# Kernel optimization log

Hardware: AMD Instinct MI355X
Metric: run time of the kernel (lower is better)

Reference implementation:

```python
import jax, jax.numpy as jnp
import numpy as np

PAD_IDX = 0
EPS = 1e-5


def make_pos(L):
    # phrase[i, j] = j - i, i.e. row i is range(-i, L-i)
    phrase = (np.arange(L)[None, :] - np.arange(L)[:, None]).astype(np.float32)
    half = int(np.ceil(L / 2))
    freq = np.linspace(0.0, L, L, dtype=np.float32)[1:half]          # [F]
    pos = freq[:, None, None] * phrase[None] / L * 2.0 * np.pi       # [F, L, L]
    pos = np.concatenate([np.cos(pos), np.sin(pos)], axis=0)        # [2F, L, L]
    return jnp.asarray(np.transpose(pos, (1, 0, 2)))                # [L, P=2F, L]


def setup_inputs() -> dict:
    key = jax.random.key(0)
    ks = jax.random.split(key, 8)
    B, L, V, D, H = 2048, 64, 4096, 64, 8
    P = 2 * (int(np.ceil(L / 2)) - 1)  # 62
    inputs = jax.random.randint(ks[0], (B, L), 0, V)
    W_emb = jax.random.normal(ks[1], (V, D), jnp.float32) * 0.02
    W_emb = W_emb.at[PAD_IDX].set(0.0)  # padding_idx row is zero
    W_qkv = jax.random.normal(ks[2], (3 * H * D, D), jnp.float32) * 0.02
    W_pos = jax.random.normal(ks[3], (P, L), jnp.float32) * 0.02
    ln_g = jnp.ones((D,), jnp.float32)
    ln_b = jnp.zeros((D,), jnp.float32)
    W1 = jax.random.normal(ks[4], (64, H), jnp.float32) * 0.1
    b1 = jnp.zeros((64,), jnp.float32)
    W2 = jax.random.normal(ks[5], (32, 64), jnp.float32) * 0.1
    b2 = jnp.zeros((32,), jnp.float32)
    return dict(inputs=inputs, W_emb=W_emb, W_qkv=W_qkv, W_pos=W_pos,
                ln_g=ln_g, ln_b=ln_b, W1=W1, b1=b1, W2=W2, b2=b2,
                n_words=4, n_names=16)


def reference(inputs, W_emb, W_qkv, W_pos, ln_g, ln_b, W1, b1, W2, b2, n_words, n_names):
    B, L = inputs.shape
    V, D = W_emb.shape
    H = W_qkv.shape[0] // (3 * D)
    pos = make_pos(L)  # [L, P, L]
    P = pos.shape[1]

    # compute_qkv: per-char q/k/v tables, then gather per token.
    qkv = (W_emb @ W_qkv.T).reshape(V, 3 * H, D)
    q, k, v = qkv[:, :H], qkv[:, H:2 * H], qkv[:, 2 * H:]
    q_t = jnp.take(q, inputs, axis=0)  # [B, L, H, D]
    k_t = jnp.take(k, inputs, axis=0)
    v_t = jnp.take(v, inputs, axis=0)

    # Equivalent to gathering char_sim[h, ids, ids]: qkv is a per-token linear,
    # so q[ids] @ k[ids]^T == char_sim.index_select(1, ids).index_select(-1, ids).
    sim = jnp.einsum('blhd,bmhd->bhlm', q_t, k_t) / jnp.sqrt(jnp.float32(D))
    key_pad = (inputs == PAD_IDX)[:, None, None, :]
    sim = jnp.where(key_pad, jnp.float32(-1e9), sim)  # char_sim[:, :, pad_idx] = -1e9

    # positional bias: Linear(L->P) on clipped scores, contracted with pos basis.
    sim_clip = jnp.where(sim > -1e8, sim, jnp.float32(0.0))
    pos_w = jnp.einsum('bhlm,pm->bhlp', sim_clip, W_pos)        # [B, H, L, P]
    pos_bias = jnp.einsum('bhlp,lpm->bhlm', pos_w, pos) / P     # mean over P

    attn = jax.nn.softmax(sim + pos_bias, axis=-1)              # dropout p=0 -> id
    out = jnp.einsum('bhlm,bmhd->blhd', attn, v_t)              # [B, L, H, D]

    # sdpa LayerNorm over word_vec_d
    mu = out.mean(-1, keepdims=True)
    var = out.var(-1, keepdims=True)
    out = (out - mu) * jax.lax.rsqrt(var + EPS) * ln_g + ln_b

    # MLP over the head dimension: [B, L, D, H] -> [B, L, D, 32]
    ft = jnp.swapaxes(out, 2, 3)
    h1 = jax.nn.relu(jnp.einsum('bldh,oh->bldo', ft, W1) + b1)
    h2 = jnp.einsum('bldo,po->bldp', h1, W2) + b2
    char_ft = h2.reshape(B, L, -1)                              # [B, L, D*32]

    # masked mean pooling over chars -> word feature
    maskf = (inputs != PAD_IDX).astype(char_ft.dtype)
    word_ft = jnp.einsum('bl,blf->bf', maskf, char_ft) / maskf.sum(-1, keepdims=True)

    # equal-size splits: words -> names (mean) -> groups of names
    Fdim = word_ft.shape[-1]
    name_ft = word_ft.reshape(B // n_words, n_words, Fdim).mean(1)
    return name_ft.reshape(-1, n_names, Fdim)
```

## Files before the change

kernel.cpp:

```cpp
#include <hip/hip_runtime.h>
#include <hip/hip_bf16.h>


typedef __attribute__((ext_vector_type(8))) short short8;
typedef __attribute__((ext_vector_type(4))) float f32x4;

union FragU { uint4 u; short8 v; };

__device__ __forceinline__ unsigned short f2bf(float f) {
    union { float f; unsigned int i; } c; c.f = f;
    unsigned int i = c.i;
    unsigned int r = (i + 0x7fffu + ((i >> 16) & 1u)) >> 16;
    return (unsigned short)r;
}
__device__ __forceinline__ float asf(unsigned int u) {
    union { unsigned int i; float f; } c; c.i = u; return c.f;
}
__device__ __forceinline__ float bfsel(uint2 g, int i) {
    unsigned u = (i < 2) ? g.x : g.y;
    return asf((i & 1) ? (u & 0xffff0000u) : (u << 16));
}

__device__ __forceinline__ void packstore4(unsigned* rowptr, int c,
                                           float v0, float v1, float v2, float v3) {
    float p0 = __shfl_xor(v0, 1), p1 = __shfl_xor(v1, 1);
    float p2 = __shfl_xor(v2, 1), p3 = __shfl_xor(v3, 1);
    int odd = c & 1;
    unsigned a0 = odd ? ((unsigned)f2bf(p2) | ((unsigned)f2bf(v2) << 16))
                      : ((unsigned)f2bf(v0) | ((unsigned)f2bf(p0) << 16));
    unsigned a1 = odd ? ((unsigned)f2bf(p3) | ((unsigned)f2bf(v3) << 16))
                      : ((unsigned)f2bf(v1) | ((unsigned)f2bf(p1) << 16));
    int ba = (c >> 1) + (odd ? 16 : 0);
    rowptr[ba] = a0; rowptr[ba + 8] = a1;
}

__global__ __launch_bounds__(256) void k_qkv(const float* __restrict__ W_emb,
                                             const float* __restrict__ W_qkv,
                                             unsigned short* __restrict__ qkvb) {
    __shared__ float At[4096];
    __shared__ float Bt[4096];
    int t = threadIdx.x;
    int bt = blockIdx.x / 24, rt = blockIdx.x - bt * 24;
    int r = t >> 2, part = t & 3;
    const float4* esrc = (const float4*)(W_emb + (size_t)((bt << 6) + r) * 64 + part * 16);
    const float4* wsrc = (const float4*)(W_qkv + (size_t)((rt << 6) + r) * 64 + part * 16);
#pragma unroll
    for (int j = 0; j < 4; ++j) {
        float4 e4 = esrc[j], w4 = wsrc[j];
        int c0 = part * 16 + j * 4;
        At[(c0 + 0) * 64 + r] = e4.x; At[(c0 + 1) * 64 + r] = e4.y;
        At[(c0 + 2) * 64 + r] = e4.z; At[(c0 + 3) * 64 + r] = e4.w;
        Bt[(c0 + 0) * 64 + r] = w4.x; Bt[(c0 + 1) * 64 + r] = w4.y;
        Bt[(c0 + 2) * 64 + r] = w4.z; Bt[(c0 + 3) * 64 + r] = w4.w;
    }
    __syncthreads();
    int l0 = (t >> 4) << 2, m0 = (t & 15) << 2;
    float acc[4][4] = {};
#pragma unroll 4
    for (int k = 0; k < 64; ++k) {
        float4 a  = *(const float4*)(At + k * 64 + l0);
        float4 bb = *(const float4*)(Bt + k * 64 + m0);
        float aa[4] = {a.x, a.y, a.z, a.w};
        float bv[4] = {bb.x, bb.y, bb.z, bb.w};
#pragma unroll
        for (int i = 0; i < 4; ++i)
#pragma unroll
            for (int j = 0; j < 4; ++j)
                acc[i][j] = fmaf(aa[i], bv[j], acc[i][j]);
    }
#pragma unroll
    for (int i = 0; i < 4; ++i) {
        unsigned w0 = (unsigned)f2bf(acc[i][0]) | ((unsigned)f2bf(acc[i][1]) << 16);
        unsigned w1 = (unsigned)f2bf(acc[i][2]) | ((unsigned)f2bf(acc[i][3]) << 16);
        unsigned* dst = (unsigned*)(qkvb + (size_t)((bt << 6) + l0 + i) * 1536 + (rt << 6) + m0);
        dst[0] = w0; dst[1] = w1;
    }
}

__global__ void k_tab(const float* __restrict__ W_pos,
                      unsigned short* __restrict__ cst,
                      unsigned short* __restrict__ csl,
                      unsigned short* __restrict__ wpos) {
    int t = threadIdx.x;
    const float w = 6.283185307179586f / 63.0f;
    for (int e = t; e < 4096; e += 256) {
        int row = e >> 6, col = e & 63;
        {
            int j = col, x = row;
            float val = 0.0f;
            if (j < 31)       val = cosf(w * (float)(((j + 1) * x) % 63));
            else if (j >= 32 && j < 63) val = sinf(w * (float)(((j - 31) * x) % 63));
            cst[e] = f2bf(val);
        }
        {
            int j = row, x = col;
            float val = 0.0f;
            if (j < 31)       val = cosf(w * (float)(((j + 1) * x) % 63));
            else if (j >= 32 && j < 63) val = sinf(w * (float)(((j - 31) * x) % 63));
            csl[e] = f2bf(val);
        }
        {
            int j = row;
            float val = 0.0f;
            if (j < 31) val = W_pos[j * 64 + col];
            else if (j >= 32 && j < 63) val = W_pos[(j - 1) * 64 + col];
            wpos[e] = f2bf(val);
        }
    }
}

__global__ __launch_bounds__(128, 4) void k_attn(
    const int* __restrict__ inputs,
    const unsigned short* __restrict__ qkvb,
    const unsigned short* __restrict__ cstg,
    const unsigned short* __restrict__ cslg,
    const unsigned short* __restrict__ wposg,
    const float* __restrict__ ln_g,
    const float* __restrict__ ln_b,
    unsigned short* __restrict__ out_n)
{
    __shared__ __align__(16) unsigned int smem[4608];
    unsigned int* S0d = smem;
    unsigned int* S1d = smem + 2304;
    int t = threadIdx.x, w2 = t >> 6, lane = t & 63;
    int b = blockIdx.x >> 3, h = blockIdx.x & 7;
    const int* toks = inputs + b * 64;
    int r = lane & 15, q = lane >> 4, c = r;
    int tk = toks[lane];
    int mt0 = 2 * w2;

    int mk[4]; float gvv[4], bvv[4];
#pragma unroll
    for (int nt = 0; nt < 4; ++nt) {
        mk[nt] = (toks[16 * nt + c] == 0);
        gvv[nt] = ln_g[16 * nt + c];
        bvv[nt] = ln_b[16 * nt + c];
    }

    {
        const uint4* src = (const uint4*)(qkvb + (size_t)tk * 1536 + (w2 ? 512 : 0) + h * 64);
        uint4* dst = (uint4*)((w2 ? S1d : S0d) + lane * 36);
#pragma unroll
        for (int j = 0; j < 8; ++j) dst[j] = src[j];
    }
    __syncthreads();

    f32x4 sc[2][4], acc[2][4];
    const f32x4 zf = {0.f, 0.f, 0.f, 0.f};

#pragma unroll
    for (int u = 0; u < 2; ++u)
#pragma unroll
        for (int nt = 0; nt < 4; ++nt) sc[u][nt] = zf;
#pragma unroll
    for (int ks = 0; ks < 2; ++ks) {
        FragU Af[2], Bf[4];
#pragma unroll
        for (int u = 0; u < 2; ++u)
            Af[u].u = *(const uint4*)(S0d + (16 * (mt0 + u) + r) * 36 + 16 * ks + 4 * q);
#pragma unroll
        for (int nt = 0; nt < 4; ++nt)
            Bf[nt].u = *(const uint4*)(S1d + (16 * nt + r) * 36 + 16 * ks + 4 * q);
#pragma unroll
        for (int u = 0; u < 2; ++u)
#pragma unroll
            for (int nt = 0; nt < 4; ++nt)
                sc[u][nt] = __builtin_amdgcn_mfma_f32_16x16x32_bf16(Af[u].v, Bf[nt].v, sc[u][nt], 0, 0, 0);
    }
#pragma unroll
    for (int u = 0; u < 2; ++u) {
#pragma unroll
        for (int nt = 0; nt < 4; ++nt) {
            f32x4 vv = sc[u][nt];
#pragma unroll
            for (int i = 0; i < 4; ++i) vv[i] = mk[nt] ? 0.0f : vv[i] * 0.125f;
            sc[u][nt] = vv;
        }
#pragma unroll
        for (int i = 0; i < 4; ++i) {
            int l = 16 * (mt0 + u) + 4 * q + i;
            packstore4(S0d + l * 36, c, sc[u][0][i], sc[u][1][i], sc[u][2][i], sc[u][3][i]);
        }
    }
    __syncthreads();

#pragma unroll
    for (int u = 0; u < 2; ++u)
#pragma unroll
        for (int nt = 0; nt < 4; ++nt) acc[u][nt] = zf;
#pragma unroll
    for (int ks = 0; ks < 2; ++ks) {
        FragU Af[2], Bf[4];
#pragma unroll
        for (int u = 0; u < 2; ++u)
            Af[u].u = *(const uint4*)(S0d + (16 * (mt0 + u) + r) * 36 + 16 * ks + 4 * q);
#pragma unroll
        for (int nt = 0; nt < 4; ++nt)
            Bf[nt].u = *(const uint4*)(wposg + (16 * nt + r) * 64 + 32 * ks + 8 * q);
#pragma unroll
        for (int u = 0; u < 2; ++u)
#pragma unroll
            for (int nt = 0; nt < 4; ++nt)
                acc[u][nt] = __builtin_amdgcn_mfma_f32_16x16x32_bf16(Af[u].v, Bf[nt].v, acc[u][nt], 0, 0, 0);
    }
#pragma unroll
    for (int u = 0; u < 2; ++u) {
        int mt = mt0 + u;
        uint2 t00 = *(const uint2*)(cslg + (c) * 64 + 16 * mt + 4 * q);
        uint2 t01 = *(const uint2*)(cslg + (32 + c) * 64 + 16 * mt + 4 * q);
        uint2 t10 = *(const uint2*)(cslg + (16 + c) * 64 + 16 * mt + 4 * q);
        uint2 t11 = *(const uint2*)(cslg + (48 + c) * 64 + 16 * mt + 4 * q);
#pragma unroll
        for (int i = 0; i < 4; ++i) {
            int l = 16 * mt + 4 * q + i;
            float cv0 = bfsel(t00, i), sv0 = bfsel(t01, i);
            float cv1 = bfsel(t10, i), sv1 = bfsel(t11, i);
            float pc0 = acc[u][0][i], ps0 = acc[u][2][i];
            float pc1 = acc[u][1][i], ps1 = acc[u][3][i];
            float u0 = pc0 * cv0 - ps0 * sv0;
            float u1 = pc1 * cv1 - ps1 * sv1;
            float u2 = pc0 * sv0 + ps0 * cv0;
            float u3 = pc1 * sv1 + ps1 * cv1;
            packstore4(S1d + l * 36, c, u0, u1, u2, u3);
        }
    }

#pragma unroll
    for (int u = 0; u < 2; ++u)
#pragma unroll
        for (int nt = 0; nt < 4; ++nt) acc[u][nt] = zf;
#pragma unroll
    for (int ks = 0; ks < 2; ++ks) {
        FragU Af[2], Bf[4];
#pragma unroll
        for (int u = 0; u < 2; ++u)
            Af[u].u = *(const uint4*)(S1d + (16 * (mt0 + u) + r) * 36 + 16 * ks + 4 * q);
#pragma unroll
        for (int nt = 0; nt < 4; ++nt)
            Bf[nt].u = *(const uint4*)(cstg + (16 * nt + r) * 64 + 32 * ks + 8 * q);
#pragma unroll
        for (int u = 0; u < 2; ++u)
#pragma unroll
            for (int nt = 0; nt < 4; ++nt)
                acc[u][nt] = __builtin_amdgcn_mfma_f32_16x16x32_bf16(Af[u].v, Bf[nt].v, acc[u][nt], 0, 0, 0);
    }

    uint4 V4[4];
    {
        const uint4* vsrc = (const uint4*)(qkvb + (size_t)tk * 1536 + 1024 + h * 64 + 32 * w2);
#pragma unroll
        for (int j = 0; j < 4; ++j) V4[j] = vsrc[j];
    }

#pragma unroll
    for (int u = 0; u < 2; ++u)
#pragma unroll
        for (int i = 0; i < 4; ++i) {
            int l = 16 * (mt0 + u) + 4 * q + i;
            float e0 = mk[0] ? 0.f : __expf(fmaf(acc[u][0][i], 1.0f / 62.0f, sc[u][0][i]));
            float e1 = mk[1] ? 0.f : __expf(fmaf(acc[u][1][i], 1.0f / 62.0f, sc[u][1][i]));
            float e2 = mk[2] ? 0.f : __expf(fmaf(acc[u][2][i], 1.0f / 62.0f, sc[u][2][i]));
            float e3 = mk[3] ? 0.f : __expf(fmaf(acc[u][3][i], 1.0f / 62.0f, sc[u][3][i]));
            float s = e0 + e1 + e2 + e3;
            s += __shfl_xor(s, 1);
            s += __shfl_xor(s, 2);
            s += __shfl_xor(s, 4);
            s += __shfl_xor(s, 8);
            float inv = 1.0f / s;
            packstore4(S0d + l * 36, c, e0 * inv, e1 * inv, e2 * inv, e3 * inv);
        }

    {
        int odd = lane & 1;
        const unsigned* Vd = (const unsigned*)V4;
#pragma unroll
        for (int jj = 0; jj < 16; ++jj) {
            unsigned my = Vd[jj];
            unsigned pr = __shfl_xor(my, 1);
            unsigned val = odd ? ((pr >> 16) | (my & 0xffff0000u))
                               : ((my & 0xffffu) | (pr << 16));
            S1d[(32 * w2 + 2 * jj + odd) * 36 + (lane >> 1)] = val;
        }
    }
    __syncthreads();

#pragma unroll
    for (int u = 0; u < 2; ++u)
#pragma unroll
        for (int nt = 0; nt < 4; ++nt) acc[u][nt] = zf;
#pragma unroll
    for (int ks = 0; ks < 2; ++ks) {
        FragU Af[2], Bf[4];
#pragma unroll
        for (int u = 0; u < 2; ++u)
            Af[u].u = *(const uint4*)(S0d + (16 * (mt0 + u) + r) * 36 + 16 * ks + 4 * q);
#pragma unroll
        for (int nt = 0; nt < 4; ++nt)
            Bf[nt].u = *(const uint4*)(S1d + (16 * nt + r) * 36 + 16 * ks + 4 * q);
#pragma unroll
        for (int u = 0; u < 2; ++u)
#pragma unroll
            for (int nt = 0; nt < 4; ++nt)
                acc[u][nt] = __builtin_amdgcn_mfma_f32_16x16x32_bf16(Af[u].v, Bf[nt].v, acc[u][nt], 0, 0, 0);
    }
    {
        unsigned* outw = (unsigned*)out_n;
        size_t hb = ((size_t)b * 8 + h) * 64;
#pragma unroll
        for (int u = 0; u < 2; ++u)
#pragma unroll
            for (int i = 0; i < 4; ++i) {
                int l = 16 * (mt0 + u) + 4 * q + i;
                float v0 = acc[u][0][i], v1 = acc[u][1][i], v2 = acc[u][2][i], v3 = acc[u][3][i];
                float s1 = v0 + v1 + v2 + v3;
                float s2 = v0 * v0 + v1 * v1 + v2 * v2 + v3 * v3;
                s1 += __shfl_xor(s1, 1); s2 += __shfl_xor(s2, 1);
                s1 += __shfl_xor(s1, 2); s2 += __shfl_xor(s2, 2);
                s1 += __shfl_xor(s1, 4); s2 += __shfl_xor(s2, 4);
                s1 += __shfl_xor(s1, 8); s2 += __shfl_xor(s2, 8);
                float mu = s1 * (1.0f / 64.0f);
                float var = s2 * (1.0f / 64.0f) - mu * mu;
                float rstd = rsqrtf(var + 1e-5f);
                float y0 = (v0 - mu) * rstd * gvv[0] + bvv[0];
                float y1 = (v1 - mu) * rstd * gvv[1] + bvv[1];
                float y2 = (v2 - mu) * rstd * gvv[2] + bvv[2];
                float y3 = (v3 - mu) * rstd * gvv[3] + bvv[3];
                packstore4(outw + (hb + l) * 32, c, y0, y1, y2, y3);
            }
    }
}

__global__ __launch_bounds__(256) void k_mlp(const int* __restrict__ inputs,
                                             const unsigned short* __restrict__ out_n,
                                             const float* __restrict__ W1,
                                             const float* __restrict__ b1,
                                             float* __restrict__ gws) {
    __shared__ unsigned short XT[8320];
    __shared__ float wl[64];
    int t = threadIdx.x, w = t >> 6, lane = t & 63;
    int b = blockIdx.x;
    int ot = w >> 1, dt = w & 1;
    int kq = lane >> 4, n = lane & 15;

    if (t < 64) {
        int tok = inputs[b * 64 + t];
        unsigned long long bal = __ballot(tok != 0);
        int cnt = __popcll(bal);
        if (cnt < 1) cnt = 1;
        wl[t] = (tok != 0) ? 1.0f / (float)cnt : 0.0f;
    }

    FragU Wf[2];
    float b1v[2];
#pragma unroll
    for (int om = 0; om < 2; ++om) {
        int o = 32 * ot + 16 * om + n;
        b1v[om] = b1[o];
        if (kq == 0) {
            const float4* wsrc = (const float4*)(W1 + o * 8);
            float4 wa = wsrc[0], wb = wsrc[1];
            Wf[om].u.x = (unsigned)f2bf(wa.x) | ((unsigned)f2bf(wa.y) << 16);
            Wf[om].u.y = (unsigned)f2bf(wa.z) | ((unsigned)f2bf(wa.w) << 16);
            Wf[om].u.z = (unsigned)f2bf(wb.x) | ((unsigned)f2bf(wb.y) << 16);
            Wf[om].u.w = (unsigned)f2bf(wb.z) | ((unsigned)f2bf(wb.w) << 16);
        } else {
            Wf[om].u = make_uint4(0, 0, 0, 0);
        }
    }

    f32x4 racc[2][2];
    const f32x4 zf = {0.f, 0.f, 0.f, 0.f};
#pragma unroll
    for (int dm = 0; dm < 2; ++dm)
#pragma unroll
        for (int om = 0; om < 2; ++om) racc[dm][om] = zf;

    int lh = t & 7;
    int lr = (t >> 3) & 15;
    int half = t >> 7;

    for (int cc = 0; cc < 4; ++cc) {
        __syncthreads();
        {
            const unsigned short* src = out_n + (size_t)b * 32768 + lh * 4096
                                        + (16 * cc + lr) * 64 + half * 32;
            unsigned short* dst = XT + lr * 520 + lh;
#pragma unroll
            for (int j = 0; j < 4; ++j) {
                uint4 u = ((const uint4*)src)[j];
                int d0 = half * 32 + j * 8;
                dst[(d0 + 0) * 8] = (unsigned short)(u.x & 0xffffu);
                dst[(d0 + 1) * 8] = (unsigned short)(u.x >> 16);
                dst[(d0 + 2) * 8] = (unsigned short)(u.y & 0xffffu);
                dst[(d0 + 3) * 8] = (unsigned short)(u.y >> 16);
                dst[(d0 + 4) * 8] = (unsigned short)(u.z & 0xffffu);
                dst[(d0 + 5) * 8] = (unsigned short)(u.z >> 16);
                dst[(d0 + 6) * 8] = (unsigned short)(u.w & 0xffffu);
                dst[(d0 + 7) * 8] = (unsigned short)(u.w >> 16);
            }
        }
        __syncthreads();
#pragma unroll 4
        for (int l = 0; l < 16; ++l) {
            FragU Xf[2];
#pragma unroll
            for (int dm = 0; dm < 2; ++dm) {
                if (kq == 0)
                    Xf[dm].u = *(const uint4*)(XT + l * 520 + (32 * dt + 16 * dm + n) * 8);
                else
                    Xf[dm].u = make_uint4(0, 0, 0, 0);
            }
            float wv = wl[16 * cc + l];
#pragma unroll
            for (int dm = 0; dm < 2; ++dm)
#pragma unroll
                for (int om = 0; om < 2; ++om) {
                    f32x4 C = __builtin_amdgcn_mfma_f32_16x16x32_bf16(Xf[dm].v, Wf[om].v, zf, 0, 0, 0);
#pragma unroll
                    for (int i = 0; i < 4; ++i)
                        racc[dm][om][i] = fmaf(wv, fmaxf(C[i] + b1v[om], 0.0f), racc[dm][om][i]);
                }
        }
    }
    float* gb = gws + (size_t)b * 4096;
#pragma unroll
    for (int dm = 0; dm < 2; ++dm)
#pragma unroll
        for (int om = 0; om < 2; ++om) {
            int o = 32 * ot + 16 * om + n;
#pragma unroll
            for (int i = 0; i < 4; ++i) {
                int d = 32 * dt + 16 * dm + 4 * kq + i;
                gb[d * 64 + o] = racc[dm][om][i];
            }
        }
}

__global__ __launch_bounds__(256) void k_final(const float* __restrict__ gws,
                                               const float* __restrict__ W2,
                                               const float* __restrict__ b2,
                                               float* __restrict__ out) {
    __shared__ float gbar[4096];
    __shared__ float w2s[32 * 68];
    __shared__ float b2s[32];
    int t = threadIdx.x;
    int n = blockIdx.x;
    for (int e = t; e < 4096; e += 256) {
        size_t base = (size_t)(4 * n) * 4096 + e;
        gbar[e] = 0.25f * (gws[base] + gws[base + 4096] + gws[base + 8192] + gws[base + 12288]);
    }
    for (int e = t; e < 2048; e += 256) {
        int p = e >> 6, o = e & 63;
        w2s[p * 68 + o] = W2[e];
    }
    if (t < 32) b2s[t] = b2[t];
    __syncthreads();
#pragma unroll
    for (int jj = 0; jj < 8; ++jj) {
        int f = jj * 256 + t;
        int d = f >> 5, p = f & 31;
        float acc = b2s[p];
        for (int o4 = 0; o4 < 16; ++o4) {
            float4 gvv = *(const float4*)(gbar + d * 64 + o4 * 4);
            float4 wv = *(const float4*)(w2s + p * 68 + o4 * 4);
            acc = fmaf(gvv.x, wv.x, acc);
            acc = fmaf(gvv.y, wv.y, acc);
            acc = fmaf(gvv.z, wv.z, acc);
            acc = fmaf(gvv.w, wv.w, acc);
        }
        out[(size_t)n * 2048 + f] = acc;
    }
}

extern "C" void kernel_launch(void* const* d_in, const int* in_sizes, int n_in,
                              void* d_out, int out_size, void* d_ws, size_t ws_size,
                              hipStream_t stream) {
    const int*   inputs = (const int*)d_in[0];
    const float* W_emb  = (const float*)d_in[1];
    const float* W_qkv  = (const float*)d_in[2];
    const float* W_pos  = (const float*)d_in[3];
    const float* ln_g   = (const float*)d_in[4];
    const float* ln_b   = (const float*)d_in[5];
    const float* W1     = (const float*)d_in[6];
    const float* b1     = (const float*)d_in[7];
    const float* W2     = (const float*)d_in[8];
    const float* b2     = (const float*)d_in[9];
    float* out = (float*)d_out;

    unsigned short* qkvb = (unsigned short*)d_ws;
    unsigned short* cst  = qkvb + 6291456;
    unsigned short* csl  = cst + 4096;
    unsigned short* wpos = csl + 4096;
    float* gws = (float*)(wpos + 4096);
    unsigned short* out_n = (unsigned short*)(gws + 8388608);

    hipLaunchKernelGGL(k_qkv,   dim3(64 * 24), dim3(256), 0, stream, W_emb, W_qkv, qkvb);
    hipLaunchKernelGGL(k_tab,   dim3(1),       dim3(256), 0, stream, W_pos, cst, csl, wpos);
    hipLaunchKernelGGL(k_attn,  dim3(16384),   dim3(128), 0, stream,
                       inputs, qkvb, cst, csl, wpos, ln_g, ln_b, out_n);
    hipLaunchKernelGGL(k_mlp,   dim3(2048),    dim3(256), 0, stream, inputs, out_n, W1, b1, gws);
    hipLaunchKernelGGL(k_final, dim3(512),     dim3(256), 0, stream, gws, W2, b2, out);
}
```

Before: 398.6 us.

## Swizzle attention LDS, defer softmax normalization, stage coalesced output, merge prep kernels

Replaces the padded 36-dword LDS row stride in the attention kernel with an XOR-swizzled 32-dword layout, shrinking shared memory and raising the occupancy hint from 4 to 5 blocks. Softmax normalization is deferred: unnormalized exponentials feed the PV MFMA and the row sum is folded into the LayerNorm epsilon, which works because LayerNorm is scale-invariant. The final output is staged through LDS and written with coalesced 16-byte stores instead of scattered 32-bit stores. The table kernel is merged into the QKV kernel as one extra block, removing a launch. It adds an extra barrier and risks small numeric differences from the rescaled epsilon.

```diff
diff --git a/kernel.cpp b/kernel.cpp
--- a/kernel.cpp
+++ b/kernel.cpp
@@ -20,26 +20,68 @@
     unsigned u = (i < 2) ? g.x : g.y;
     return asf((i & 1) ? (u & 0xffff0000u) : (u << 16));
 }
-
-__device__ __forceinline__ void packstore4(unsigned* rowptr, int c,
+__device__ __forceinline__ unsigned pk2(float lo, float hi) {
+    return (unsigned)f2bf(lo) | ((unsigned)f2bf(hi) << 16);
+}
+
+__device__ __forceinline__ int swzi(int row, int dw4) {
+    return (row << 5) + (dw4 ^ ((row & 7) << 2));
+}
+__device__ __forceinline__ int swzs(int row, int dw) {
+    return (row << 5) + (((dw & ~3) ^ ((row & 7) << 2)) | (dw & 3));
+}
+
+__device__ __forceinline__ void packstore4(unsigned* S, int row, int c,
                                            float v0, float v1, float v2, float v3) {
     float p0 = __shfl_xor(v0, 1), p1 = __shfl_xor(v1, 1);
     float p2 = __shfl_xor(v2, 1), p3 = __shfl_xor(v3, 1);
     int odd = c & 1;
-    unsigned a0 = odd ? ((unsigned)f2bf(p2) | ((unsigned)f2bf(v2) << 16))
-                      : ((unsigned)f2bf(v0) | ((unsigned)f2bf(p0) << 16));
-    unsigned a1 = odd ? ((unsigned)f2bf(p3) | ((unsigned)f2bf(v3) << 16))
-                      : ((unsigned)f2bf(v1) | ((unsigned)f2bf(p1) << 16));
+    float x0 = odd ? p2 : v0, y0 = odd ? v2 : p0;
+    float x1 = odd ? p3 : v1, y1 = odd ? v3 : p1;
+    unsigned a0 = pk2(x0, y0), a1 = pk2(x1, y1);
     int ba = (c >> 1) + (odd ? 16 : 0);
-    rowptr[ba] = a0; rowptr[ba + 8] = a1;
-}
-
-__global__ __launch_bounds__(256) void k_qkv(const float* __restrict__ W_emb,
+    S[swzs(row, ba)] = a0;
+    S[swzs(row, ba + 8)] = a1;
+}
+
+__global__ __launch_bounds__(256) void k_pre(const float* __restrict__ W_emb,
                                              const float* __restrict__ W_qkv,
-                                             unsigned short* __restrict__ qkvb) {
+                                             const float* __restrict__ W_pos,
+                                             unsigned short* __restrict__ qkvb,
+                                             unsigned short* __restrict__ cst,
+                                             unsigned short* __restrict__ csl,
+                                             unsigned short* __restrict__ wpos) {
     __shared__ float At[4096];
     __shared__ float Bt[4096];
     int t = threadIdx.x;
+    if (blockIdx.x >= 1536) {
+        const float w = 6.283185307179586f / 63.0f;
+        for (int e = t; e < 4096; e += 256) {
+            int row = e >> 6, col = e & 63;
+            {
+                int j = col, x = row;
+                float val = 0.0f;
+                if (j < 31)       val = cosf(w * (float)(((j + 1) * x) % 63));
+                else if (j >= 32 && j < 63) val = sinf(w * (float)(((j - 31) * x) % 63));
+                cst[e] = f2bf(val);
+            }
+            {
+                int j = row, x = col;
+                float val = 0.0f;
+                if (j < 31)       val = cosf(w * (float)(((j + 1) * x) % 63));
+                else if (j >= 32 && j < 63) val = sinf(w * (float)(((j - 31) * x) % 63));
+                csl[e] = f2bf(val);
+            }
+            {
+                int j = row;
+                float val = 0.0f;
+                if (j < 31) val = W_pos[j * 64 + col];
+                else if (j >= 32 && j < 63) val = W_pos[(j - 1) * 64 + col];
+                wpos[e] = f2bf(val);
+            }
+        }
+        return;
+    }
     int bt = blockIdx.x / 24, rt = blockIdx.x - bt * 24;
     int r = t >> 2, part = t & 3;
     const float4* esrc = (const float4*)(W_emb + (size_t)((bt << 6) + r) * 64 + part * 16);
@@ -70,46 +112,13 @@
     }
 #pragma unroll
     for (int i = 0; i < 4; ++i) {
-        unsigned w0 = (unsigned)f2bf(acc[i][0]) | ((unsigned)f2bf(acc[i][1]) << 16);
-        unsigned w1 = (unsigned)f2bf(acc[i][2]) | ((unsigned)f2bf(acc[i][3]) << 16);
         unsigned* dst = (unsigned*)(qkvb + (size_t)((bt << 6) + l0 + i) * 1536 + (rt << 6) + m0);
-        dst[0] = w0; dst[1] = w1;
-    }
-}
-
-__global__ void k_tab(const float* __restrict__ W_pos,
-                      unsigned short* __restrict__ cst,
-                      unsigned short* __restrict__ csl,
-                      unsigned short* __restrict__ wpos) {
-    int t = threadIdx.x;
-    const float w = 6.283185307179586f / 63.0f;
-    for (int e = t; e < 4096; e += 256) {
-        int row = e >> 6, col = e & 63;
-        {
-            int j = col, x = row;
-            float val = 0.0f;
-            if (j < 31)       val = cosf(w * (float)(((j + 1) * x) % 63));
-            else if (j >= 32 && j < 63) val = sinf(w * (float)(((j - 31) * x) % 63));
-            cst[e] = f2bf(val);
-        }
-        {
-            int j = row, x = col;
-            float val = 0.0f;
-            if (j < 31)       val = cosf(w * (float)(((j + 1) * x) % 63));
-            else if (j >= 32 && j < 63) val = sinf(w * (float)(((j - 31) * x) % 63));
-            csl[e] = f2bf(val);
-        }
-        {
-            int j = row;
-            float val = 0.0f;
-            if (j < 31) val = W_pos[j * 64 + col];
-            else if (j >= 32 && j < 63) val = W_pos[(j - 1) * 64 + col];
-            wpos[e] = f2bf(val);
-        }
-    }
-}
-
-__global__ __launch_bounds__(128, 4) void k_attn(
+        dst[0] = pk2(acc[i][0], acc[i][1]);
+        dst[1] = pk2(acc[i][2], acc[i][3]);
+    }
+}
+
+__global__ __launch_bounds__(128, 5) void k_attn(
     const int* __restrict__ inputs,
     const unsigned short* __restrict__ qkvb,
     const unsigned short* __restrict__ cstg,
@@ -119,9 +128,9 @@
     const float* __restrict__ ln_b,
     unsigned short* __restrict__ out_n)
 {
-    __shared__ __align__(16) unsigned int smem[4608];
+    __shared__ __align__(16) unsigned int smem[4096];
     unsigned int* S0d = smem;
-    unsigned int* S1d = smem + 2304;
+    unsigned int* S1d = smem + 2048;
     int t = threadIdx.x, w2 = t >> 6, lane = t & 63;
     int b = blockIdx.x >> 3, h = blockIdx.x & 7;
     const int* toks = inputs + b * 64;
@@ -139,9 +148,10 @@
 
     {
         const uint4* src = (const uint4*)(qkvb + (size_t)tk * 1536 + (w2 ? 512 : 0) + h * 64);
-        uint4* dst = (uint4*)((w2 ? S1d : S0d) + lane * 36);
-#pragma unroll
-        for (int j = 0; j < 8; ++j) dst[j] = src[j];
+        unsigned* Sd = w2 ? S1d : S0d;
+#pragma unroll
+        for (int j = 0; j < 8; ++j)
+            *(uint4*)(Sd + swzi(lane, 4 * j)) = src[j];
     }
     __syncthreads();
 
@@ -157,10 +167,10 @@
         FragU Af[2], Bf[4];
 #pragma unroll
         for (int u = 0; u < 2; ++u)
-            Af[u].u = *(const uint4*)(S0d + (16 * (mt0 + u) + r) * 36 + 16 * ks + 4 * q);
+            Af[u].u = *(const uint4*)(S0d + swzi(16 * (mt0 + u) + r, 16 * ks + 4 * q));
 #pragma unroll
         for (int nt = 0; nt < 4; ++nt)
-            Bf[nt].u = *(const uint4*)(S1d + (16 * nt + r) * 36 + 16 * ks + 4 * q);
+            Bf[nt].u = *(const uint4*)(S1d + swzi(16 * nt + r, 16 * ks + 4 * q));
 #pragma unroll
         for (int u = 0; u < 2; ++u)
 #pragma unroll
@@ -179,7 +189,7 @@
 #pragma unroll
         for (int i = 0; i < 4; ++i) {
             int l = 16 * (mt0 + u) + 4 * q + i;
-            packstore4(S0d + l * 36, c, sc[u][0][i], sc[u][1][i], sc[u][2][i], sc[u][3][i]);
+            packstore4(S0d, l, c, sc[u][0][i], sc[u][1][i], sc[u][2][i], sc[u][3][i]);
         }
     }
     __syncthreads();
@@ -193,7 +203,7 @@
         FragU Af[2], Bf[4];
 #pragma unroll
         for (int u = 0; u < 2; ++u)
-            Af[u].u = *(const uint4*)(S0d + (16 * (mt0 + u) + r) * 36 + 16 * ks + 4 * q);
+            Af[u].u = *(const uint4*)(S0d + swzi(16 * (mt0 + u) + r, 16 * ks + 4 * q));
 #pragma unroll
         for (int nt = 0; nt < 4; ++nt)
             Bf[nt].u = *(const uint4*)(wposg + (16 * nt + r) * 64 + 32 * ks + 8 * q);
@@ -221,7 +231,7 @@
             float u1 = pc1 * cv1 - ps1 * sv1;
             float u2 = pc0 * sv0 + ps0 * cv0;
             float u3 = pc1 * sv1 + ps1 * cv1;
-            packstore4(S1d + l * 36, c, u0, u1, u2, u3);
+            packstore4(S1d, l, c, u0, u1, u2, u3);
         }
     }
 
@@ -234,7 +244,7 @@
         FragU Af[2], Bf[4];
 #pragma unroll
         for (int u = 0; u < 2; ++u)
-            Af[u].u = *(const uint4*)(S1d + (16 * (mt0 + u) + r) * 36 + 16 * ks + 4 * q);
+            Af[u].u = *(const uint4*)(S1d + swzi(16 * (mt0 + u) + r, 16 * ks + 4 * q));
 #pragma unroll
         for (int nt = 0; nt < 4; ++nt)
             Bf[nt].u = *(const uint4*)(cstg + (16 * nt + r) * 64 + 32 * ks + 8 * q);
@@ -252,6 +262,7 @@
         for (int j = 0; j < 4; ++j) V4[j] = vsrc[j];
     }
 
+    float rs[2][4];
 #pragma unroll
     for (int u = 0; u < 2; ++u)
 #pragma unroll
@@ -266,8 +277,8 @@
             s += __shfl_xor(s, 2);
             s += __shfl_xor(s, 4);
             s += __shfl_xor(s, 8);
-            float inv = 1.0f / s;
-            packstore4(S0d + l * 36, c, e0 * inv, e1 * inv, e2 * inv, e3 * inv);
+            rs[u][i] = s;
+            packstore4(S0d, l, c, e0, e1, e2, e3);
         }
 
     {
@@ -279,7 +290,7 @@
             unsigned pr = __shfl_xor(my, 1);
             unsigned val = odd ? ((pr >> 16) | (my & 0xffff0000u))
                                : ((my & 0xffffu) | (pr << 16));
-            S1d[(32 * w2 + 2 * jj + odd) * 36 + (lane >> 1)] = val;
+            S1d[swzs(32 * w2 + 2 * jj + odd, lane >> 1)] = val;
         }
     }
     __syncthreads();
@@ -293,40 +304,49 @@
         FragU Af[2], Bf[4];
 #pragma unroll
         for (int u = 0; u < 2; ++u)
-            Af[u].u = *(const uint4*)(S0d + (16 * (mt0 + u) + r) * 36 + 16 * ks + 4 * q);
+            Af[u].u = *(const uint4*)(S0d + swzi(16 * (mt0 + u) + r, 16 * ks + 4 * q));
 #pragma unroll
         for (int nt = 0; nt < 4; ++nt)
-            Bf[nt].u = *(const uint4*)(S1d + (16 * nt + r) * 36 + 16 * ks + 4 * q);
+            Bf[nt].u = *(const uint4*)(S1d + swzi(16 * nt + r, 16 * ks + 4 * q));
 #pragma unroll
         for (int u = 0; u < 2; ++u)
 #pragma unroll
             for (int nt = 0; nt < 4; ++nt)
                 acc[u][nt] = __builtin_amdgcn_mfma_f32_16x16x32_bf16(Af[u].v, Bf[nt].v, acc[u][nt], 0, 0, 0);
     }
+    __syncthreads();
+
+#pragma unroll
+    for (int u = 0; u < 2; ++u)
+#pragma unroll
+        for (int i = 0; i < 4; ++i) {
+            int l = 16 * (mt0 + u) + 4 * q + i;
+            float v0 = acc[u][0][i], v1 = acc[u][1][i], v2 = acc[u][2][i], v3 = acc[u][3][i];
+            float s1 = v0 + v1 + v2 + v3;
+            float s2 = v0 * v0 + v1 * v1 + v2 * v2 + v3 * v3;
+            s1 += __shfl_xor(s1, 1); s2 += __shfl_xor(s2, 1);
+            s1 += __shfl_xor(s1, 2); s2 += __shfl_xor(s2, 2);
+            s1 += __shfl_xor(s1, 4); s2 += __shfl_xor(s2, 4);
+            s1 += __shfl_xor(s1, 8); s2 += __shfl_xor(s2, 8);
+            float mu = s1 * (1.0f / 64.0f);
+            float var = s2 * (1.0f / 64.0f) - mu * mu;
+            float ss = rs[u][i];
+            float rstd = rsqrtf(fmaf(ss * ss, 1e-5f, var));
+            float y0 = (v0 - mu) * rstd * gvv[0] + bvv[0];
+            float y1 = (v1 - mu) * rstd * gvv[1] + bvv[1];
+            float y2 = (v2 - mu) * rstd * gvv[2] + bvv[2];
+            float y3 = (v3 - mu) * rstd * gvv[3] + bvv[3];
+            packstore4(S1d, l, c, y0, y1, y2, y3);
+        }
+
     {
         unsigned* outw = (unsigned*)out_n;
         size_t hb = ((size_t)b * 8 + h) * 64;
-#pragma unroll
-        for (int u = 0; u < 2; ++u)
-#pragma unroll
-            for (int i = 0; i < 4; ++i) {
-                int l = 16 * (mt0 + u) + 4 * q + i;
-                float v0 = acc[u][0][i], v1 = acc[u][1][i], v2 = acc[u][2][i], v3 = acc[u][3][i];
-                float s1 = v0 + v1 + v2 + v3;
-                float s2 = v0 * v0 + v1 * v1 + v2 * v2 + v3 * v3;
-                s1 += __shfl_xor(s1, 1); s2 += __shfl_xor(s2, 1);
-                s1 += __shfl_xor(s1, 2); s2 += __shfl_xor(s2, 2);
-                s1 += __shfl_xor(s1, 4); s2 += __shfl_xor(s2, 4);
-                s1 += __shfl_xor(s1, 8); s2 += __shfl_xor(s2, 8);
-                float mu = s1 * (1.0f / 64.0f);
-                float var = s2 * (1.0f / 64.0f) - mu * mu;
-                float rstd = rsqrtf(var + 1e-5f);
-                float y0 = (v0 - mu) * rstd * gvv[0] + bvv[0];
-                float y1 = (v1 - mu) * rstd * gvv[1] + bvv[1];
-                float y2 = (v2 - mu) * rstd * gvv[2] + bvv[2];
-                float y3 = (v3 - mu) * rstd * gvv[3] + bvv[3];
-                packstore4(outw + (hb + l) * 32, c, y0, y1, y2, y3);
-            }
+        int row = 32 * w2 + (lane >> 1), half = lane & 1;
+        unsigned* orow = outw + (hb + row) * 32 + half * 16;
+#pragma unroll
+        for (int j = 0; j < 4; ++j)
+            *(uint4*)(orow + 4 * j) = *(const uint4*)(S1d + swzi(row, half * 16 + 4 * j));
     }
 }
 
@@ -359,10 +379,10 @@
         if (kq == 0) {
             const float4* wsrc = (const float4*)(W1 + o * 8);
             float4 wa = wsrc[0], wb = wsrc[1];
-            Wf[om].u.x = (unsigned)f2bf(wa.x) | ((unsigned)f2bf(wa.y) << 16);
-            Wf[om].u.y = (unsigned)f2bf(wa.z) | ((unsigned)f2bf(wa.w) << 16);
-            Wf[om].u.z = (unsigned)f2bf(wb.x) | ((unsigned)f2bf(wb.y) << 16);
-            Wf[om].u.w = (unsigned)f2bf(wb.z) | ((unsigned)f2bf(wb.w) << 16);
+            Wf[om].u.x = pk2(wa.x, wa.y);
+            Wf[om].u.y = pk2(wa.z, wa.w);
+            Wf[om].u.z = pk2(wb.x, wb.y);
+            Wf[om].u.w = pk2(wb.z, wb.w);
         } else {
             Wf[om].u = make_uint4(0, 0, 0, 0);
         }
@@ -494,10 +514,10 @@
     float* gws = (float*)(wpos + 4096);
     unsigned short* out_n = (unsigned short*)(gws + 8388608);
 
-    hipLaunchKernelGGL(k_qkv,   dim3(64 * 24), dim3(256), 0, stream, W_emb, W_qkv, qkvb);
-    hipLaunchKernelGGL(k_tab,   dim3(1),       dim3(256), 0, stream, W_pos, cst, csl, wpos);
-    hipLaunchKernelGGL(k_attn,  dim3(16384),   dim3(128), 0, stream,
+    hipLaunchKernelGGL(k_pre,   dim3(1537),  dim3(256), 0, stream,
+                       W_emb, W_qkv, W_pos, qkvb, cst, csl, wpos);
+    hipLaunchKernelGGL(k_attn,  dim3(16384), dim3(128), 0, stream,
                        inputs, qkvb, cst, csl, wpos, ln_g, ln_b, out_n);
-    hipLaunchKernelGGL(k_mlp,   dim3(2048),    dim3(256), 0, stream, inputs, out_n, W1, b1, gws);
-    hipLaunchKernelGGL(k_final, dim3(512),     dim3(256), 0, stream, gws, W2, b2, out);
-}
+    hipLaunchKernelGGL(k_mlp,   dim3(2048),  dim3(256), 0, stream, inputs, out_n, W1, b1, gws);
+    hipLaunchKernelGGL(k_final, dim3(512),   dim3(256), 0, stream, gws, W2, b2, out);
+}
```

Measured after the change: 453.1 us. 13.7% more time.
